# Kernel tuning notes

Measured on AMD Instinct MI355X. Metric: run time of the kernel, lower is better.

Reference implementation:

```python
import jax, jax.numpy as jnp
import numpy as np

EPS = 1e-7  # K.epsilon()
ATTN_WIDTH = 12
B, L, D = 8, 4096, 768


def setup_inputs() -> dict:
    key = jax.random.key(0)
    k1, k2 = jax.random.split(key)
    x = jax.random.normal(k1, (B, L, D), dtype=jnp.float32)
    Wa = jax.random.normal(k2, (D, 1), dtype=jnp.float32) * 0.05  # RandomNormal(stddev=0.05)
    return {"x": x, "Wa": Wa}


def reference(x, Wa):
    """Banded rank-1 self-attention.

    e[b,i,j] = u[b,i]*u[b,j] with u = x @ Wa, masked to the trailing band
    i-w+1 <= j <= i, normalized by the row sum (+eps), then v = a @ x.
    Because e is rank-1 inside the band, we never materialize the LxL matrix:
      wsum_i  = sum_{j=i-w+1}^{i} u_j          (windowed cumsum)
      wvec_i  = sum_{j=i-w+1}^{i} u_j * x_j    (windowed cumsum of u*x)
      v_i     = u_i * wvec_i / (u_i * wsum_i + eps)
    which is exactly e/(sum(e)+eps) @ x.
    """
    w = ATTN_WIDTH
    u = jnp.einsum('bld,do->bl', x, Wa)            # [B, L]
    cu = jnp.cumsum(u, axis=1)                      # [B, L]
    cux = jnp.cumsum(u[..., None] * x, axis=1)      # [B, L, D]
    # shifted[i] = cu[i-w] (0 for i < w)
    cu_shift = jnp.pad(cu, ((0, 0), (w, 0)))[:, :L]
    cux_shift = jnp.pad(cux, ((0, 0), (w, 0), (0, 0)))[:, :L, :]
    wsum = cu - cu_shift                            # [B, L]
    wvec = cux - cux_shift                          # [B, L, D]
    denom = u * wsum + EPS                          # [B, L]
    v = (u[..., None] * wvec) / denom[..., None]    # [B, L, D]
    return v
```

## Files before the change

### kernel.cpp

```cpp
#include <hip/hip_runtime.h>

namespace {
constexpr int kB = 8;
constexpr int kL = 4096;
constexpr int kD = 768;
constexpr int kW = 12;
constexpr int kHalo = kW - 1;
constexpr int kT = 32;
constexpr int kRows = kT + kHalo;
constexpr int kThreads = 192;
constexpr float kEps = 1e-7f;
constexpr int kChunks = kL / kT;
constexpr int kRing = 16;
}

typedef float vfloat4 __attribute__((ext_vector_type(4)));

__global__ __launch_bounds__(kThreads, 3) void SelfAttention_banded_kernel(
    const float* __restrict__ x, const float* __restrict__ Wa,
    float* __restrict__ out) {
  __shared__ double s_part[kRows][3];
  __shared__ double s_u[kRows];
  __shared__ float s_uf[kRows];
  __shared__ float s_scale[kT];

  const int blk = blockIdx.x;
  const int b = blk / kChunks;
  const int i0 = (blk % kChunks) * kT;
  const float* xb = x + (size_t)b * kL * kD;
  float* ob = out + (size_t)b * kL * kD;

  const int tid = threadIdx.x;
  const int lane = tid & 63;
  const int wv = tid >> 6;
  const int c0 = 4 * tid;

  const vfloat4 w4 = *(const vfloat4*)(Wa + c0);

#pragma unroll 4
  for (int r = 0; r < kRows; ++r) {
    const int row = i0 - kHalo + r;
    double p = 0.0;
    if (row >= 0) {
      const vfloat4 xv = *(const vfloat4*)(xb + (size_t)row * kD + c0);
      p = (double)xv.x * (double)w4.x + (double)xv.y * (double)w4.y +
          (double)xv.z * (double)w4.z + (double)xv.w * (double)w4.w;
    }
#pragma unroll
    for (int s = 32; s >= 1; s >>= 1) p += __shfl_xor(p, s, 64);
    if (lane == 0) s_part[r][wv] = p;
  }
  __syncthreads();

  if (tid < kRows) {
    const double u = s_part[tid][0] + s_part[tid][1] + s_part[tid][2];
    s_u[tid] = u;
    s_uf[tid] = (float)u;
  }
  __syncthreads();

  if (tid < kT) {
    const double u = s_u[tid + kHalo];
    double wsum = 0.0;
#pragma unroll
    for (int k = 0; k < kW; ++k) wsum += s_u[tid + k];
    s_scale[tid] = (float)(u / (u * wsum + (double)kEps));
  }
  __syncthreads();

  float uf[kRows];
#pragma unroll
  for (int r = 0; r < kRows; ++r) uf[r] = s_uf[r];

  vfloat4 ring[kRing];
#pragma unroll
  for (int k = 0; k < kHalo; ++k) {
    const int row = i0 - kHalo + k;
    vfloat4 v = {0.f, 0.f, 0.f, 0.f};
    if (row >= 0) v = *(const vfloat4*)(xb + (size_t)row * kD + c0);
    ring[(k + kRing - kHalo) & (kRing - 1)] = v;
  }

#pragma unroll
  for (int t = 0; t < kT; ++t) {
    const int i = i0 + t;
    ring[t & (kRing - 1)] = *(const vfloat4*)(xb + (size_t)i * kD + c0);
    vfloat4 acc = {0.f, 0.f, 0.f, 0.f};
#pragma unroll
    for (int j = 0; j < kW; ++j) {
      const float u = uf[t + kHalo - j];
      const vfloat4 xv = ring[(t - j) & (kRing - 1)];
      acc.x += u * xv.x; acc.y += u * xv.y;
      acc.z += u * xv.z; acc.w += u * xv.w;
    }
    const float sc = s_scale[t];
    vfloat4 o;
    o.x = sc * acc.x; o.y = sc * acc.y;
    o.z = sc * acc.z; o.w = sc * acc.w;
    __builtin_nontemporal_store(o, (vfloat4*)(ob + (size_t)i * kD + c0));
  }
}

extern "C" void kernel_launch(void* const* d_in, const int* in_sizes, int n_in,
                              void* d_out, int out_size, void* d_ws, size_t ws_size,
                              hipStream_t stream) {
  const float* x = (const float*)d_in[0];
  const float* Wa = (const float*)d_in[1];
  float* out = (float*)d_out;
  const int grid = kB * kChunks;
  SelfAttention_banded_kernel<<<grid, kThreads, 0, stream>>>(x, Wa, out);
}
```

Measured before the change: 200.3 us.

## Split u projection into separate kernel and shrink banded tile

Computes the projection u = x·Wa in a standalone kernel that writes fp64 values to workspace. A second kernel reads u to build per-row scales and the windowed weighted sum over 16-row tiles. This removes the serial in-block reduction and sync phases from the main kernel, at the cost of an extra full read of x and a second launch.

```diff
diff --git a/kernel.cpp b/kernel.cpp
--- a/kernel.cpp
+++ b/kernel.cpp
@@ -1,4 +1,6 @@
 #include <hip/hip_runtime.h>
+
+typedef float vfloat4 __attribute__((ext_vector_type(4)));
 
 namespace {
 constexpr int kB = 8;
@@ -6,97 +8,122 @@
 constexpr int kD = 768;
 constexpr int kW = 12;
 constexpr int kHalo = kW - 1;
-constexpr int kT = 32;
-constexpr int kRows = kT + kHalo;
-constexpr int kThreads = 192;
 constexpr float kEps = 1e-7f;
-constexpr int kChunks = kL / kT;
-constexpr int kRing = 16;
+
+constexpr int kRowsPerBlockU = 16;
+constexpr int kGridU = kB * kL / kRowsPerBlockU;
+
+constexpr int kT2 = 16;
+constexpr int kRows2 = kT2 + kHalo;
+constexpr int kThreads2 = 192;
+constexpr int kChunks2 = kL / kT2;
+constexpr int kGridV = kB * kChunks2;
 }
 
-typedef float vfloat4 __attribute__((ext_vector_type(4)));
+__global__ __launch_bounds__(256, 4) void compute_u_kernel(
+    const float* __restrict__ x, const float* __restrict__ Wa,
+    double* __restrict__ u) {
+  const int lane = threadIdx.x & 63;
+  const int wv = threadIdx.x >> 6;
+  const int rg0 = blockIdx.x * kRowsPerBlockU + wv * 4;
 
-__global__ __launch_bounds__(kThreads, 3) void SelfAttention_banded_kernel(
-    const float* __restrict__ x, const float* __restrict__ Wa,
+  vfloat4 w[3];
+#pragma unroll
+  for (int k = 0; k < 3; ++k)
+    w[k] = *(const vfloat4*)(Wa + 4 * lane + 256 * k);
+
+  vfloat4 xv[4][3];
+#pragma unroll
+  for (int q = 0; q < 4; ++q)
+#pragma unroll
+    for (int k = 0; k < 3; ++k)
+      xv[q][k] = *(const vfloat4*)(x + (size_t)(rg0 + q) * kD + 4 * lane + 256 * k);
+
+  double acc[4];
+#pragma unroll
+  for (int q = 0; q < 4; ++q) {
+    double p = 0.0;
+#pragma unroll
+    for (int k = 0; k < 3; ++k) {
+      p += (double)xv[q][k].x * (double)w[k].x + (double)xv[q][k].y * (double)w[k].y +
+           (double)xv[q][k].z * (double)w[k].z + (double)xv[q][k].w * (double)w[k].w;
+    }
+    acc[q] = p;
+  }
+#pragma unroll
+  for (int q = 0; q < 4; ++q) {
+#pragma unroll
+    for (int s = 32; s >= 1; s >>= 1) acc[q] += __shfl_xor(acc[q], s, 64);
+  }
+  if (lane == 0) {
+#pragma unroll
+    for (int q = 0; q < 4; ++q) u[rg0 + q] = acc[q];
+  }
+}
+
+__global__ __launch_bounds__(kThreads2, 3) void banded_v_kernel(
+    const float* __restrict__ x, const double* __restrict__ u,
     float* __restrict__ out) {
-  __shared__ double s_part[kRows][3];
-  __shared__ double s_u[kRows];
-  __shared__ float s_uf[kRows];
-  __shared__ float s_scale[kT];
+  __shared__ float s_uf[kRows2];
+  __shared__ float s_scale[kT2];
 
   const int blk = blockIdx.x;
-  const int b = blk / kChunks;
-  const int i0 = (blk % kChunks) * kT;
+  const int b = blk / kChunks2;
+  const int i0 = (blk % kChunks2) * kT2;
   const float* xb = x + (size_t)b * kL * kD;
   float* ob = out + (size_t)b * kL * kD;
+  const double* ub = u + (size_t)b * kL;
+  const int tid = threadIdx.x;
 
-  const int tid = threadIdx.x;
-  const int lane = tid & 63;
-  const int wv = tid >> 6;
-  const int c0 = 4 * tid;
-
-  const vfloat4 w4 = *(const vfloat4*)(Wa + c0);
-
-#pragma unroll 4
-  for (int r = 0; r < kRows; ++r) {
-    const int row = i0 - kHalo + r;
-    double p = 0.0;
-    if (row >= 0) {
-      const vfloat4 xv = *(const vfloat4*)(xb + (size_t)row * kD + c0);
-      p = (double)xv.x * (double)w4.x + (double)xv.y * (double)w4.y +
-          (double)xv.z * (double)w4.z + (double)xv.w * (double)w4.w;
+  if (tid < kRows2) {
+    const int row = i0 - kHalo + tid;
+    s_uf[tid] = (row >= 0) ? (float)ub[row] : 0.0f;
+  } else if (tid >= 64 && tid < 64 + kT2) {
+    const int t = tid - 64;
+    const int i = i0 + t;
+    double wsum = 0.0;
+#pragma unroll
+    for (int k = 0; k < kW; ++k) {
+      const int j = i - kHalo + k;
+      if (j >= 0) wsum += ub[j];
     }
-#pragma unroll
-    for (int s = 32; s >= 1; s >>= 1) p += __shfl_xor(p, s, 64);
-    if (lane == 0) s_part[r][wv] = p;
+    const double uu = ub[i];
+    s_scale[t] = (float)(uu / (uu * wsum + (double)kEps));
   }
   __syncthreads();
 
-  if (tid < kRows) {
-    const double u = s_part[tid][0] + s_part[tid][1] + s_part[tid][2];
-    s_u[tid] = u;
-    s_uf[tid] = (float)u;
-  }
-  __syncthreads();
+  float uf[kRows2];
+#pragma unroll
+  for (int r = 0; r < kRows2; ++r) uf[r] = s_uf[r];
+  float sc[kT2];
+#pragma unroll
+  for (int t = 0; t < kT2; ++t) sc[t] = s_scale[t];
 
-  if (tid < kT) {
-    const double u = s_u[tid + kHalo];
-    double wsum = 0.0;
+  const int c0 = 4 * tid;
+  vfloat4 ring[kW];
 #pragma unroll
-    for (int k = 0; k < kW; ++k) wsum += s_u[tid + k];
-    s_scale[tid] = (float)(u / (u * wsum + (double)kEps));
-  }
-  __syncthreads();
-
-  float uf[kRows];
-#pragma unroll
-  for (int r = 0; r < kRows; ++r) uf[r] = s_uf[r];
-
-  vfloat4 ring[kRing];
-#pragma unroll
-  for (int k = 0; k < kHalo; ++k) {
-    const int row = i0 - kHalo + k;
+  for (int r = 0; r < kHalo; ++r) {
+    const int row = i0 - kHalo + r;
     vfloat4 v = {0.f, 0.f, 0.f, 0.f};
     if (row >= 0) v = *(const vfloat4*)(xb + (size_t)row * kD + c0);
-    ring[(k + kRing - kHalo) & (kRing - 1)] = v;
+    ring[r] = v;
   }
 
 #pragma unroll
-  for (int t = 0; t < kT; ++t) {
+  for (int t = 0; t < kT2; ++t) {
     const int i = i0 + t;
-    ring[t & (kRing - 1)] = *(const vfloat4*)(xb + (size_t)i * kD + c0);
+    const int r = kHalo + t;
+    ring[r % kW] = *(const vfloat4*)(xb + (size_t)i * kD + c0);
     vfloat4 acc = {0.f, 0.f, 0.f, 0.f};
 #pragma unroll
     for (int j = 0; j < kW; ++j) {
-      const float u = uf[t + kHalo - j];
-      const vfloat4 xv = ring[(t - j) & (kRing - 1)];
-      acc.x += u * xv.x; acc.y += u * xv.y;
-      acc.z += u * xv.z; acc.w += u * xv.w;
+      const float uu = uf[r - j];
+      const vfloat4 xv = ring[(r - j) % kW];
+      acc.x += uu * xv.x; acc.y += uu * xv.y;
+      acc.z += uu * xv.z; acc.w += uu * xv.w;
     }
-    const float sc = s_scale[t];
-    vfloat4 o;
-    o.x = sc * acc.x; o.y = sc * acc.y;
-    o.z = sc * acc.z; o.w = sc * acc.w;
+    const float s = sc[t];
+    vfloat4 o = {s * acc.x, s * acc.y, s * acc.z, s * acc.w};
     __builtin_nontemporal_store(o, (vfloat4*)(ob + (size_t)i * kD + c0));
   }
 }
@@ -107,6 +134,8 @@
   const float* x = (const float*)d_in[0];
   const float* Wa = (const float*)d_in[1];
   float* out = (float*)d_out;
-  const int grid = kB * kChunks;
-  SelfAttention_banded_kernel<<<grid, kThreads, 0, stream>>>(x, Wa, out);
+  double* u = (double*)d_ws;
+
+  compute_u_kernel<<<kGridU, 256, 0, stream>>>(x, Wa, u);
+  banded_v_kernel<<<kGridV, kThreads2, 0, stream>>>(x, u, out);
 }
```

Result: no change. 198.9 us (-0.7%).
